# Optimization experiments

Hardware: AMD Instinct MI355X
Metric: run time of the kernel (lower is better)

Reference implementation:

```python
import jax, jax.numpy as jnp
import numpy as np

K = 32                      # nsample (neighbors)
NPTS = [4096, 2048, 1024]   # npts // downsample_ratios [1,2,4]
CH = [(6, 64, 64), (134, 128, 128), (262, 256, 256)]  # (c_in_edge, c_mid, c_out) per EdgeConv
OUT_CH = 128
EPS = 1e-5


def setup_inputs():
    key = jax.random.key(0)
    ks = iter(jax.random.split(key, 64))
    d = {"pcd": jax.random.normal(next(ks), (8, 4096, 3), dtype=jnp.float32)}
    for li, (cin, cmid, cout) in enumerate(CH, start=1):
        d[f"W{li}a"] = jax.random.normal(next(ks), (cmid, cin), dtype=jnp.float32) * 0.05
        d[f"b{li}a"] = jax.random.normal(next(ks), (cmid,), dtype=jnp.float32) * 0.01
        d[f"g{li}a"] = jnp.ones((cmid,), dtype=jnp.float32)
        d[f"be{li}a"] = jnp.zeros((cmid,), dtype=jnp.float32)
        d[f"W{li}b"] = jax.random.normal(next(ks), (cout, cmid), dtype=jnp.float32) * 0.05
        d[f"b{li}b"] = jax.random.normal(next(ks), (cout,), dtype=jnp.float32) * 0.01
        d[f"g{li}b"] = jnp.ones((cout,), dtype=jnp.float32)
        d[f"be{li}b"] = jnp.zeros((cout,), dtype=jnp.float32)
    d["fcW"] = jax.random.normal(next(ks), (OUT_CH, CH[-1][2]), dtype=jnp.float32) * 0.05
    d["fcb"] = jnp.zeros((OUT_CH,), dtype=jnp.float32)
    return d


def _knn_idx(q, p, k):
    # q: [B,m,3] queries, p: [B,n,3] points -> [B,m,k] nearest-neighbor indices
    d = (jnp.sum(q * q, -1)[:, :, None] + jnp.sum(p * p, -1)[:, None, :]
         - 2.0 * jnp.einsum('bmd,bnd->bmn', q, p))
    _, idx = jax.lax.top_k(-d, k)
    return idx


def _bn(x, g, b):
    # training-mode BatchNorm2d over [B,C,m,k], biased variance (torch behavior)
    mu = jnp.mean(x, axis=(0, 2, 3), keepdims=True)
    var = jnp.mean((x - mu) ** 2, axis=(0, 2, 3), keepdims=True)
    return (x - mu) * jax.lax.rsqrt(var + EPS) * g[None, :, None, None] + b[None, :, None, None]


def _edge_conv(xyz, feat, npoints, params):
    # xyz: [B,n,3], feat: [B,C,n] or None. Range sampling = first npoints points.
    W1, b1, g1, be1, W2, b2, g2, be2 = params
    new_xyz = xyz[:, :npoints]
    # use_xyz=True: concat features (as [B,n,C]) with xyz
    f = xyz if feat is None else jnp.concatenate([jnp.transpose(feat, (0, 2, 1)), xyz], -1)
    new_f = f[:, :npoints]                       # [B,m,D]
    idx = _knn_idx(new_xyz, xyz, K)              # [B,m,K]
    knn_f = jax.vmap(lambda a, i: a[i])(f, idx)  # [B,m,K,D] gather
    tiled = jnp.broadcast_to(new_f[:, :, None, :], knn_f.shape)
    e = jnp.concatenate([knn_f - tiled, tiled], -1)  # [B,m,K,2D] edge features
    h = jnp.einsum('bmkc,oc->bomk', e, W1) + b1[None, :, None, None]
    h = jax.nn.relu(_bn(h, g1, be1))
    h = jnp.einsum('bcmk,oc->bomk', h, W2) + b2[None, :, None, None]
    h = jax.nn.relu(_bn(h, g2, be2))
    return new_xyz, jnp.max(h, axis=-1)          # max-pool over K -> [B,C,m]


def reference(pcd, W1a, b1a, g1a, be1a, W1b, b1b, g1b, be1b,
              W2a, b2a, g2a, be2a, W2b, b2b, g2b, be2b,
              W3a, b3a, g3a, be3a, W3b, b3b, g3b, be3b, fcW, fcb):
    xyz = pcd[..., :3]
    feat = None  # pcd has only xyz channels
    layer_params = [
        (W1a, b1a, g1a, be1a, W1b, b1b, g1b, be1b),
        (W2a, b2a, g2a, be2a, W2b, b2b, g2b, be2b),
        (W3a, b3a, g3a, be3a, W3b, b3b, g3b, be3b),
    ]
    for npoints, p in zip(NPTS, layer_params):
        xyz, feat = _edge_conv(xyz, feat, npoints, p)
    out_feat = jnp.einsum('bcn,oc->bon', feat, fcW) + fcb[None, :, None]
    # Range sampling: idx chain of aranges composes to arange(NPTS[-1])
    idx = jnp.broadcast_to(jnp.arange(NPTS[-1]), (pcd.shape[0], NPTS[-1]))
    return xyz, out_feat, idx, feat
```

## Files before the change

### kernel.cpp

```cpp
#include <hip/hip_runtime.h>
#include <hip/hip_bf16.h>

#define B8 8
#define KNN 32
typedef unsigned short u16;
typedef unsigned int u32;
typedef unsigned long long u64;

typedef __attribute__((ext_vector_type(8))) _Float16 half8;
typedef __attribute__((ext_vector_type(4))) float f32x4;

static __device__ __forceinline__ u16 f2h_u(float f) {
  _Float16 h = (_Float16)f; u16 u; __builtin_memcpy(&u, &h, 2); return u;
}
static __device__ __forceinline__ float h2f_u(u16 u) {
  _Float16 h; __builtin_memcpy(&h, &u, 2); return (float)h;
}

static __device__ __forceinline__ u64 enc_key(float d, int id) {
  u32 u = __float_as_uint(d);
  u = (d >= 0.f) ? (u | 0x80000000u) : ~u;
  return ((u64)u << 32) | (u32)id;
}
static __device__ __forceinline__ float dec_val(u64 k) {
  u32 u = (u32)(k >> 32);
  u = (u & 0x80000000u) ? (u & 0x7fffffffu) : ~u;
  return __uint_as_float(u);
}

static __device__ __forceinline__ u64 rank64(u64 mk, int lane, u64* slk, u64* outk, float& tau) {
  slk[lane] = mk;
  int r = 0;
#pragma unroll 16
  for (int j = 0; j < 64; ++j) r += (slk[j] < mk) ? 1 : 0;
  outk[r] = mk;
  u64 res = outk[lane];
  tau = dec_val(outk[31]);
  return res;
}

static __device__ __forceinline__ void bn_from_red(int o, const float* red_s, const float* red_q,
                                                   const float* g, const float* be, float invcnt,
                                                   float* scs, float* shs) {
  float s = 0.f, q = 0.f;
#pragma unroll
  for (int i = 0; i < 16; ++i) { s += red_s[i * 256 + o]; q += red_q[i * 256 + o]; }
  float mu  = s * invcnt;
  float var = fmaxf(q * invcnt - mu * mu, 0.f);
  float scv = g[o] * rsqrtf(var + 1e-5f);
  scs[o] = scv;
  shs[o] = fmaf(-mu, scv, be[o]);
}

__global__ __launch_bounds__(256) void knn_dual(const float* __restrict__ pcd,
                                                int* __restrict__ idx1, int* __restrict__ idx3) {
  __shared__ float4 pts[1024];
  __shared__ u64 bufk[4][32];
  __shared__ u64 slk[4][64];
  __shared__ u64 outk[4][64];
  const int t = threadIdx.x;
  const int lane = t & 63, w = t >> 6;
  const int b = blockIdx.y;
  int N, M, bx; int* idxout;
  if (blockIdx.x < 1024) { N = 4096; M = 4096; bx = blockIdx.x; idxout = idx1; }
  else                   { N = 2048; M = 1024; bx = blockIdx.x - 1024; idxout = idx3; }
  const int m = bx * 4 + w;
  const float* base = pcd + (size_t)b * 12288;
  const float qx = base[m*3], qy = base[m*3+1], qz = base[m*3+2];
  const float ax = -2.f*qx, ay = -2.f*qy, az = -2.f*qz;

  u64 heldk; float tau; int cnt = 0;

  for (int i = t; i < 1024; i += 256) {
    const float* p = base + (size_t)i * 3;
    float x = p[0], y = p[1], z = p[2];
    pts[i] = make_float4(x, y, z, x*x + y*y + z*z);
  }
  __syncthreads();

  {
    float4 p = pts[lane];
    float r0 = fmaf(ax, p.x, fmaf(ay, p.y, fmaf(az, p.z, p.w)));
    heldk = rank64(enc_key(r0, lane), lane, slk[w], outk[w], tau);
  }

  for (int n0 = 0; n0 < N; n0 += 1024) {
    if (n0) {
      __syncthreads();
      for (int i = t; i < 1024; i += 256) {
        const float* p = base + (size_t)(n0 + i) * 3;
        float x = p[0], y = p[1], z = p[2];
        pts[i] = make_float4(x, y, z, x*x + y*y + z*z);
      }
      __syncthreads();
    }
    for (int c = 0; c < 1024; c += 256) {
      float4 p0 = pts[c + lane];
      float4 p1 = pts[c + 64 + lane];
      float4 p2 = pts[c + 128 + lane];
      float4 p3 = pts[c + 192 + lane];
      float r[4];
      r[0] = fmaf(ax, p0.x, fmaf(ay, p0.y, fmaf(az, p0.z, p0.w)));
      r[1] = fmaf(ax, p1.x, fmaf(ay, p1.y, fmaf(az, p1.z, p1.w)));
      r[2] = fmaf(ax, p2.x, fmaf(ay, p2.y, fmaf(az, p2.z, p2.w)));
      r[3] = fmaf(ax, p3.x, fmaf(ay, p3.y, fmaf(az, p3.z, p3.w)));
      if (n0 == 0 && c == 0) r[0] = 3.4e38f;
      float rmn = fminf(fminf(r[0], r[1]), fminf(r[2], r[3]));
      if (!__any(rmn < tau)) continue;
#pragma unroll
      for (int j = 0; j < 4; ++j) {
        float rr = r[j];
        if (!__any(rr < tau)) continue;
        int gid = n0 + c + j * 64 + lane;
        bool pass = rr < tau;
        while (__any(pass)) {
          u64 mk_ = __ballot(pass);
          int before = __popcll(mk_ & ((1ull << lane) - 1ull));
          int total  = __popcll(mk_);
          int room = 32 - cnt;
          if (pass && before < room) {
            bufk[w][cnt + before] = enc_key(rr, gid);
            pass = false;
          }
          if (total >= room) {
            u64 mk = (lane < 32) ? heldk : bufk[w][lane - 32];
            heldk = rank64(mk, lane, slk[w], outk[w], tau);
            cnt = 0;
            pass = pass && (rr < tau);
          } else {
            cnt += total;
          }
        }
      }
    }
  }
  if (cnt > 0) {
    int bl = lane - 32;
    u64 mk = (lane < 32) ? heldk
             : ((bl < cnt) ? bufk[w][bl]
                           : ((0xFFFFFFFFull << 32) | (0xFFFFFF00u | (u32)lane)));
    heldk = rank64(mk, lane, slk[w], outk[w], tau);
  }
  if (lane < KNN) idxout[((size_t)b * M + m) * KNN + lane] = (int)(u32)(heldk & 0xFFFFFFFFu);
}

__global__ void prep_all(
    const float* __restrict__ W1a, const float* __restrict__ W1b,
    const float* __restrict__ W2a, const float* __restrict__ W2b,
    const float* __restrict__ W3a, const float* __restrict__ W3b,
    float* __restrict__ RED,
    float* __restrict__ WAT1, float* __restrict__ WBT1, u16* __restrict__ WBH1,
    float* __restrict__ WBT2, u16* __restrict__ WAH2, u16* __restrict__ WBH2,
    float* __restrict__ WBT3, u16* __restrict__ WAH3, u16* __restrict__ WBH3)
{
  int i0 = blockIdx.x * 256 + threadIdx.x;
  int NT = gridDim.x * 256;
  for (int i = i0; i < 49152; i += NT) RED[i] = 0.f;
  for (int i = i0; i < 256; i += NT) {
    int c = i >> 6, o = i & 63;
    float w1 = (c < 3) ? W1a[o*6 + c] : 0.f;
    float w2 = (c < 3) ? W1a[o*6 + 3 + c] : 0.f;
    WAT1[i] = w1; WBT1[i] = w2 - w1;
  }
  for (int i = i0; i < 4096; i += NT) WBH1[i] = f2h_u(W1b[i]);
  for (int i = i0; i < 68*128; i += NT) {
    int c = i >> 7, o = i & 127;
    float w1 = 0.f, w2 = 0.f;
    if (c < 67) { w1 = W2a[o*134 + c]; w2 = W2a[o*134 + 67 + c]; }
    WBT2[i] = w2 - w1;
  }
  for (int i = i0; i < 128*128; i += NT) {
    int o = i >> 7, k = i & 127;
    WAH2[i] = (k < 67) ? f2h_u(W2a[o*134 + k]) : (u16)0;
  }
  for (int i = i0; i < 16384; i += NT) WBH2[i] = f2h_u(W2b[i]);
  for (int i = i0; i < 132*256; i += NT) {
    int c = i >> 8, o = i & 255;
    float w1 = 0.f, w2 = 0.f;
    if (c < 131) { w1 = W3a[o*262 + c]; w2 = W3a[o*262 + 131 + c]; }
    WBT3[i] = w2 - w1;
  }
  for (int i = i0; i < 256*192; i += NT) {
    int o = i / 192, k = i - o * 192;
    WAH3[i] = (k < 131) ? f2h_u(W3a[o*262 + k]) : (u16)0;
  }
  for (int i = i0; i < 65536; i += NT) WBH3[i] = f2h_u(W3b[i]);
}

template<int C2, int CM, int MODE, int F16>
__global__ __launch_bounds__(256) void conv_a_gemm(
    const void* __restrict__ F, int frs, size_t fbstride,
    const int* __restrict__ idx,
    const float* __restrict__ Wt,
    const float* __restrict__ bias,
    const float* __restrict__ T,
    float* __restrict__ Tout,
    float* __restrict__ red_s, float* __restrict__ red_q,
    int M)
{
  constexpr int KP = (C2 + 3) & ~3;
  constexpr int KC = (KP <= 68) ? KP : 44;
  __shared__ float At[64][KC];
  __shared__ float Wts[KC][64];
  __shared__ int ji[64];
  __shared__ float sred[4][64];
  __shared__ float qred[4][64];
  const int t = threadIdx.x;
  const int rt = blockIdx.x, ot = blockIdx.y, b = blockIdx.z;
  const int R0 = rt * 64, oc0 = ot * 64;

  if (t < 64) {
    int gr = R0 + t;
    ji[t] = (MODE == 0) ? gr : idx[((size_t)b * M + (gr >> 5)) * KNN + (gr & 31)];
  }

  const int cg = t & 15, rg = t >> 4;
  const int r0 = rg * 4, c0 = cg * 4;
  float acc[4][4];
  if (MODE == 0) {
#pragma unroll
    for (int j = 0; j < 4; ++j) {
      float bv = bias[oc0 + c0 + j];
#pragma unroll
      for (int i = 0; i < 4; ++i) acc[i][j] = bv;
    }
  } else {
#pragma unroll
    for (int i = 0; i < 4; ++i) {
      const float* tp = T + ((size_t)b * M + (size_t)((R0 + r0 + i) >> 5)) * CM + oc0 + c0;
      acc[i][0] = tp[0]; acc[i][1] = tp[1]; acc[i][2] = tp[2]; acc[i][3] = tp[3];
    }
  }
  __syncthreads();

  for (int k0 = 0; k0 < KP; k0 += KC) {
    if (k0) __syncthreads();
    for (int i = t; i < KC * 64; i += 256) {
      int c = i >> 6, o = i & 63;
      Wts[c][o] = Wt[(size_t)(k0 + c) * CM + oc0 + o];
    }
    if constexpr (C2 == 3) {
      const float* Fb = (const float*)F + (size_t)b * fbstride;
      for (int i = t; i < 64 * 4; i += 256) {
        int r = i >> 2, c = i & 3;
        At[r][c] = (c < 3) ? Fb[(size_t)ji[r] * 3 + c] : 0.f;
      }
    } else if constexpr (F16) {
      const u16* Fb = (const u16*)F + (size_t)b * fbstride;
      constexpr int C4 = KC / 4;
      for (int i = t; i < 64 * C4; i += 256) {
        int r = i / C4, c4 = i - r * C4;
        ushort4 v = *(const ushort4*)&Fb[(size_t)ji[r] * frs + k0 + c4 * 4];
        At[r][c4*4]   = h2f_u(v.x);
        At[r][c4*4+1] = h2f_u(v.y);
        At[r][c4*4+2] = h2f_u(v.z);
        At[r][c4*4+3] = h2f_u(v.w);
      }
    } else {
      const float* Fb = (const float*)F + (size_t)b * fbstride;
      constexpr int C4 = KC / 4;
      for (int i = t; i < 64 * C4; i += 256) {
        int r = i / C4, c4 = i - r * C4;
        *(float4*)&At[r][c4 * 4] = *(const float4*)&Fb[(size_t)ji[r] * frs + k0 + c4 * 4];
      }
    }
    __syncthreads();

#pragma unroll 4
    for (int k = 0; k < KC; ++k) {
      const float4 w4 = *(const float4*)&Wts[k][c0];
      float a0 = At[r0][k], a1 = At[r0+1][k], a2 = At[r0+2][k], a3 = At[r0+3][k];
      acc[0][0]=fmaf(a0,w4.x,acc[0][0]); acc[0][1]=fmaf(a0,w4.y,acc[0][1]);
      acc[0][2]=fmaf(a0,w4.z,acc[0][2]); acc[0][3]=fmaf(a0,w4.w,acc[0][3]);
      acc[1][0]=fmaf(a1,w4.x,acc[1][0]); acc[1][1]=fmaf(a1,w4.y,acc[1][1]);
      acc[1][2]=fmaf(a1,w4.z,acc[1][2]); acc[1][3]=fmaf(a1,w4.w,acc[1][3]);
      acc[2][0]=fmaf(a2,w4.x,acc[2][0]); acc[2][1]=fmaf(a2,w4.y,acc[2][1]);
      acc[2][2]=fmaf(a2,w4.z,acc[2][2]); acc[2][3]=fmaf(a2,w4.w,acc[2][3]);
      acc[3][0]=fmaf(a3,w4.x,acc[3][0]); acc[3][1]=fmaf(a3,w4.y,acc[3][1]);
      acc[3][2]=fmaf(a3,w4.z,acc[3][2]); acc[3][3]=fmaf(a3,w4.w,acc[3][3]);
    }
  }

  if (MODE == 0) {
    float* op = Tout + ((size_t)b * M + R0) * (size_t)CM + oc0;
#pragma unroll
    for (int i = 0; i < 4; ++i) {
      float* p = op + (size_t)(r0 + i) * CM + c0;
      p[0]=acc[i][0]; p[1]=acc[i][1]; p[2]=acc[i][2]; p[3]=acc[i][3];
    }
  } else {
    float cs[4], cq_[4];
#pragma unroll
    for (int j = 0; j < 4; ++j) {
      float s = acc[0][j] + acc[1][j] + acc[2][j] + acc[3][j];
      float q = acc[0][j]*acc[0][j] + acc[1][j]*acc[1][j] + acc[2][j]*acc[2][j] + acc[3][j]*acc[3][j];
      s += __shfl_xor(s, 16); q += __shfl_xor(q, 16);
      s += __shfl_xor(s, 32); q += __shfl_xor(q, 32);
      cs[j] = s; cq_[j] = q;
    }
    const int wv = t >> 6;
    if ((t & 48) == 0) {
#pragma unroll
      for (int j = 0; j < 4; ++j) { sred[wv][c0 + j] = cs[j]; qred[wv][c0 + j] = cq_[j]; }
    }
    __syncthreads();
    if (t < 64) {
      float s = sred[0][t] + sred[1][t] + sred[2][t] + sred[3][t];
      float q = qred[0][t] + qred[1][t] + qred[2][t] + qred[3][t];
      int shdw = (rt & 15) * 256;
      atomicAdd(&red_s[shdw + t], s);
      atomicAdd(&red_q[shdw + t], q);
    }
  }
}

__global__ __launch_bounds__(256) void l1_convb(
    const float* __restrict__ pcd,
    const int* __restrict__ idx,
    const float* __restrict__ WAT,
    const float* __restrict__ T,
    const u16* __restrict__ Wbh,
    const float* __restrict__ bb,
    const float* __restrict__ gA, const float* __restrict__ beA,
    const float* __restrict__ redA_s, const float* __restrict__ redA_q,
    float* __restrict__ redB_s, float* __restrict__ redB_q,
    float* __restrict__ hmax)
{
  __shared__ u16 Alds[64][72];
  __shared__ u16 Wlds[64][72];
  __shared__ float xyzs[64][4];
  __shared__ float was[3][64];
  __shared__ float scs[64], shs[64];
  __shared__ int ji[64];
  const int t = threadIdx.x;
  const int lane = t & 63, w = t >> 6;
  const int wr = w >> 1, wc = w & 1;
  const int cl = lane & 15, rq = lane >> 4;
  const int rt = blockIdx.x, b = blockIdx.y;
  const int R0 = rt * 64;
  const float* pb = pcd + (size_t)b * 12288;

  if (t < 64) ji[t] = idx[((size_t)b * 4096 + ((R0 + t) >> 5)) * KNN + ((R0 + t) & 31)];
  if (t < 192) was[t / 64][t & 63] = WAT[t];
  if (t >= 192) bn_from_red(t - 192, redA_s, redA_q, gA, beA, 1.f/1048576.f, scs, shs);
  for (int i = t; i < 64 * 8; i += 256) {
    int o = i >> 3, seg = i & 7;
    *(float4*)&Wlds[o][seg * 8] = *(const float4*)&Wbh[(size_t)o * 64 + seg * 8];
  }
  __syncthreads();
  if (t < 64) {
    const float* p = pb + (size_t)ji[t] * 3;
    xyzs[t][0] = p[0]; xyzs[t][1] = p[1]; xyzs[t][2] = p[2]; xyzs[t][3] = 0.f;
  }
  __syncthreads();

  for (int i = t; i < 64 * 8; i += 256) {
    int r = i >> 3, seg = i & 7;
    float px = xyzs[r][0], py = xyzs[r][1], pz = xyzs[r][2];
    const float* Tm = T + ((size_t)b * 4096 + (size_t)((R0 + r) >> 5)) * 64;
    half8 ov;
#pragma unroll
    for (int j2 = 0; j2 < 8; ++j2) {
      int c = seg * 8 + j2;
      float hh = Tm[c];
      hh = fmaf(px, was[0][c], hh);
      hh = fmaf(py, was[1][c], hh);
      hh = fmaf(pz, was[2][c], hh);
      ov[j2] = (_Float16)fmaxf(0.f, fmaf(hh, scs[c], shs[c]));
    }
    *(half8*)&Alds[r][seg * 8] = ov;
  }
  __syncthreads();

  f32x4 acc[2][2];
#pragma unroll
  for (int fr = 0; fr < 2; ++fr)
#pragma unroll
    for (int fc = 0; fc < 2; ++fc) {
      float bv = bb[wc * 32 + fc * 16 + cl];
#pragma unroll
      for (int r = 0; r < 4; ++r) acc[fr][fc][r] = bv;
    }

#pragma unroll
  for (int kk = 0; kk < 2; ++kk) {
    half8 af[2], bf[2];
#pragma unroll
    for (int fr = 0; fr < 2; ++fr)
      af[fr] = *(const half8*)&Alds[wr*32 + fr*16 + cl][kk*32 + rq*8];
#pragma unroll
    for (int fc = 0; fc < 2; ++fc)
      bf[fc] = *(const half8*)&Wlds[wc*32 + fc*16 + cl][kk*32 + rq*8];
#pragma unroll
    for (int fr = 0; fr < 2; ++fr)
#pragma unroll
      for (int fc = 0; fc < 2; ++fc)
        acc[fr][fc] = __builtin_amdgcn_mfma_f32_16x16x32_f16(af[fr], bf[fc], acc[fr][fc], 0, 0, 0);
  }

#pragma unroll
  for (int fc = 0; fc < 2; ++fc) {
    float s = 0.f, q = 0.f, mx = -3.4e38f;
#pragma unroll
    for (int fr = 0; fr < 2; ++fr)
#pragma unroll
      for (int r = 0; r < 4; ++r) {
        float v = acc[fr][fc][r];
        s += v; q += v * v; mx = fmaxf(mx, v);
      }
    s += __shfl_xor(s, 16); q += __shfl_xor(q, 16); mx = fmaxf(mx, __shfl_xor(mx, 16));
    s += __shfl_xor(s, 32); q += __shfl_xor(q, 32); mx = fmaxf(mx, __shfl_xor(mx, 32));
    if (rq == 0) {
      int col = wc * 32 + fc * 16 + cl;
      int shdw = (rt & 15) * 256;
      atomicAdd(&redB_s[shdw + col], s);
      atomicAdd(&redB_q[shdw + col], q);
      hmax[((size_t)b * 4096 + (size_t)(rt * 2 + wr)) * 64 + col] = mx;
    }
  }
}

template<int CM, int KPAD>
__global__ __launch_bounds__(256) void conv_a_mfma(
    const u16* __restrict__ F, int frs, size_t fbstride,
    const int* __restrict__ idx, int idxstride,
    const u16* __restrict__ Wh,
    const float* __restrict__ T,
    u32* __restrict__ H32,
    float* __restrict__ red_s, float* __restrict__ red_q,
    int M)
{
  constexpr int FC = CM / 32;
  __shared__ u16 Alds[64][72];
  __shared__ u16 Wlds[CM][72];
  __shared__ int ji[64];
  const int t = threadIdx.x;
  const int lane = t & 63, w = t >> 6;
  const int wr = w >> 1, wc = w & 1;
  const int cl = lane & 15, rq = lane >> 4;
  const int rt = blockIdx.x, b = blockIdx.y;
  const int R0 = rt * 64;
  const u16* Fb = F + (size_t)b * fbstride;

  if (t < 64) ji[t] = idx[((size_t)b * idxstride + ((R0 + t) >> 5)) * KNN + ((R0 + t) & 31)];

  f32x4 acc[2][FC];
#pragma unroll
  for (int fr = 0; fr < 2; ++fr)
#pragma unroll
    for (int fc = 0; fc < FC; ++fc) {
      int col = wc * (CM/2) + fc * 16 + cl;
#pragma unroll
      for (int r = 0; r < 4; ++r) {
        int row = R0 + wr*32 + fr*16 + rq*4 + r;
        acc[fr][fc][r] = T[((size_t)b * M + (row >> 5)) * CM + col];
      }
    }
  __syncthreads();

  for (int k0 = 0; k0 < KPAD; k0 += 64) {
    if (k0) __syncthreads();
    for (int i = t; i < 64 * 16; i += 256) {
      int r = i >> 4, seg = i & 15;
      int k = k0 + seg * 4;
      ushort4 s = {0,0,0,0};
      if (k < frs) s = *(const ushort4*)&Fb[(size_t)ji[r] * frs + k];
      *(ushort4*)&Alds[r][seg * 4] = s;
    }
    for (int i = t; i < CM * 8; i += 256) {
      int o = i >> 3, seg = i & 7;
      *(float4*)&Wlds[o][seg * 8] = *(const float4*)&Wh[(size_t)o * KPAD + k0 + seg * 8];
    }
    __syncthreads();

#pragma unroll
    for (int kk = 0; kk < 2; ++kk) {
      half8 af[2], bf[FC];
#pragma unroll
      for (int fr = 0; fr < 2; ++fr)
        af[fr] = *(const half8*)&Alds[wr*32 + fr*16 + cl][kk*32 + rq*8];
#pragma unroll
      for (int fc = 0; fc < FC; ++fc)
        bf[fc] = *(const half8*)&Wlds[wc*(CM/2) + fc*16 + cl][kk*32 + rq*8];
#pragma unroll
      for (int fr = 0; fr < 2; ++fr)
#pragma unroll
        for (int fc = 0; fc < FC; ++fc)
          acc[fr][fc] = __builtin_amdgcn_mfma_f32_16x16x32_f16(af[fr], bf[fc], acc[fr][fc], 0, 0, 0);
    }
  }

  u32* Hb4 = H32 + ((size_t)b * ((size_t)M * KNN / 4) + (size_t)(R0 >> 2)) * CM;
#pragma unroll
  for (int fr = 0; fr < 2; ++fr)
#pragma unroll
    for (int fc = 0; fc < FC; ++fc) {
      int col = wc*(CM/2) + fc*16 + cl;
      u32 v = __builtin_amdgcn_cvt_pk_fp8_f32(acc[fr][fc][0], acc[fr][fc][1], 0, false);
      v = __builtin_amdgcn_cvt_pk_fp8_f32(acc[fr][fc][2], acc[fr][fc][3], v, true);
      Hb4[(size_t)(wr*8 + fr*4 + rq) * CM + col] = v;
    }

#pragma unroll
  for (int fc = 0; fc < FC; ++fc) {
    float s = 0.f, q = 0.f;
#pragma unroll
    for (int fr = 0; fr < 2; ++fr)
#pragma unroll
      for (int r = 0; r < 4; ++r) {
        float v = acc[fr][fc][r];
        s += v; q += v * v;
      }
    s += __shfl_xor(s, 16); q += __shfl_xor(q, 16);
    s += __shfl_xor(s, 32); q += __shfl_xor(q, 32);
    if (rq == 0) {
      int col = wc*(CM/2) + fc*16 + cl;
      int shdw = (rt & 15) * 256;
      atomicAdd(&red_s[shdw + col], s);
      atomicAdd(&red_q[shdw + col], q);
    }
  }
}

template<int CM>
__global__ __launch_bounds__(512) void conv_b_fused(
    const u32* __restrict__ H32,
    const u16* __restrict__ Wh,
    const float* __restrict__ bb,
    const float* __restrict__ gA, const float* __restrict__ beA,
    const float* __restrict__ redA_s, const float* __restrict__ redA_q, float invcnt,
    float* __restrict__ redB_s, float* __restrict__ redB_q,
    float* __restrict__ hmax,
    int Mrows)
{
  constexpr int FC = CM / 32;
  __shared__ u16 Alds[128][72];
  __shared__ u16 Wlds[CM][72];
  __shared__ float scs[CM], shs[CM];
  const int t = threadIdx.x;
  const int lane = t & 63, w = t >> 6;
  const int wr = w >> 1;
  const int wc = w & 1;
  const int cl = lane & 15, rq = lane >> 4;
  const int rt = blockIdx.x, b = blockIdx.y;
  const u32* Hb4 = H32 + ((size_t)b * ((size_t)Mrows / 4) + (size_t)(rt * 32)) * CM;

  for (int i = t; i < CM; i += 512) bn_from_red(i, redA_s, redA_q, gA, beA, invcnt, scs, shs);

  f32x4 acc[2][FC];
#pragma unroll
  for (int fr = 0; fr < 2; ++fr)
#pragma unroll
    for (int fc = 0; fc < FC; ++fc) {
      float bv = bb[wc * (CM/2) + fc * 16 + cl];
#pragma unroll
      for (int r = 0; r < 4; ++r) acc[fr][fc][r] = bv;
    }
  __syncthreads();

  for (int k0 = 0; k0 < CM; k0 += 64) {
    if (k0) __syncthreads();
    for (int i = t; i < 128 * 8; i += 512) {
      int r = i >> 3, seg = i & 7;
      int rg = r >> 2, sh8 = (r & 3) * 8;
      const u32* hp = Hb4 + (size_t)rg * CM + k0 + seg * 8;
      half8 ov;
#pragma unroll
      for (int j = 0; j < 8; ++j) {
        float v = __builtin_amdgcn_cvt_f32_fp8((hp[j] >> sh8) & 0xffu, 0);
        int c = k0 + seg * 8 + j;
        v = fmaxf(0.f, fmaf(v, scs[c], shs[c]));
        ov[j] = (_Float16)v;
      }
      *(half8*)&Alds[r][seg * 8] = ov;
    }
    for (int i = t; i < CM * 8; i += 512) {
      int o = i >> 3, seg = i & 7;
      *(float4*)&Wlds[o][seg * 8] = *(const float4*)&Wh[(size_t)o * CM + k0 + seg * 8];
    }
    __syncthreads();

#pragma unroll
    for (int kk = 0; kk < 2; ++kk) {
      half8 af[2], bf[FC];
#pragma unroll
      for (int fr = 0; fr < 2; ++fr)
        af[fr] = *(const half8*)&Alds[wr*32 + fr*16 + cl][kk*32 + rq*8];
#pragma unroll
      for (int fc = 0; fc < FC; ++fc)
        bf[fc] = *(const half8*)&Wlds[wc*(CM/2) + fc*16 + cl][kk*32 + rq*8];
#pragma unroll
      for (int fr = 0; fr < 2; ++fr)
#pragma unroll
        for (int fc = 0; fc < FC; ++fc)
          acc[fr][fc] = __builtin_amdgcn_mfma_f32_16x16x32_f16(af[fr], bf[fc], acc[fr][fc], 0, 0, 0);
    }
  }

#pragma unroll
  for (int fc = 0; fc < FC; ++fc) {
    float s = 0.f, q = 0.f, mx = -3.4e38f;
#pragma unroll
    for (int fr = 0; fr < 2; ++fr)
#pragma unroll
      for (int r = 0; r < 4; ++r) {
        float v = acc[fr][fc][r];
        s += v; q += v * v; mx = fmaxf(mx, v);
      }
    s += __shfl_xor(s, 16); q += __shfl_xor(q, 16); mx = fmaxf(mx, __shfl_xor(mx, 16));
    s += __shfl_xor(s, 32); q += __shfl_xor(q, 32); mx = fmaxf(mx, __shfl_xor(mx, 32));
    if (rq == 0) {
      int col = wc*(CM/2) + fc*16 + cl;
      int shdw = (rt & 15) * 256;
      atomicAdd(&redB_s[shdw + col], s);
      atomicAdd(&redB_q[shdw + col], q);
      hmax[((size_t)b * (Mrows >> 5) + (size_t)(rt * 4 + wr)) * CM + col] = mx;
    }
  }
}

__global__ __launch_bounds__(256) void bnrelu_fb(const float* __restrict__ hm,
    const float* __restrict__ gB, const float* __restrict__ beB,
    const float* __restrict__ redB_s, const float* __restrict__ redB_q, float invcnt,
    const float* __restrict__ pcd,
    u16* __restrict__ fout, int CM, int fostride, size_t fobstride, int M) {
  __shared__ float scs[256], shs[256];
  for (int o = threadIdx.x; o < CM; o += 256) bn_from_red(o, redB_s, redB_q, gB, beB, invcnt, scs, shs);
  __syncthreads();
  int i = blockIdx.x * 256 + threadIdx.x;
  int cq = CM >> 2;
  int total = B8 * M * cq;
  if (i >= total) return;
  int c4 = i % cq; int r = i / cq;
  int b = r / M, m = r - b * M;
  float4 v = *(const float4*)&hm[((size_t)b * M + m) * CM + c4 * 4];
  int c = c4 * 4;
  ushort4 o;
  o.x = f2h_u(fmaxf(0.f, fmaf(v.x, scs[c],   shs[c])));
  o.y = f2h_u(fmaxf(0.f, fmaf(v.y, scs[c+1], shs[c+1])));
  o.z = f2h_u(fmaxf(0.f, fmaf(v.z, scs[c+2], shs[c+2])));
  o.w = f2h_u(fmaxf(0.f, fmaf(v.w, scs[c+3], shs[c+3])));
  u16* op = fout + (size_t)b * fobstride + (size_t)m * fostride;
  *(ushort4*)(op + c) = o;
  if (pcd && c4 == 0) {
    const float* p = pcd + ((size_t)b * 4096 + m) * 3;
    half8 xz;
    xz[0] = (_Float16)p[0]; xz[1] = (_Float16)p[1]; xz[2] = (_Float16)p[2];
    xz[3] = (_Float16)0.f; xz[4] = (_Float16)0.f; xz[5] = (_Float16)0.f;
    xz[6] = (_Float16)0.f; xz[7] = (_Float16)0.f;
    *(half8*)(op + CM) = xz;
  }
}

__global__ __launch_bounds__(256) void fc_fused(
    const float* __restrict__ hm,
    const float* __restrict__ gB, const float* __restrict__ beB,
    const float* __restrict__ redB_s, const float* __restrict__ redB_q, float invcnt,
    const float* __restrict__ fcW, const float* __restrict__ fcb,
    const float* __restrict__ pcd,
    float* __restrict__ out0, float* __restrict__ out1,
    float* __restrict__ out2, float* __restrict__ out3) {
  __shared__ float tile[32 * 257];
  __shared__ float scs[256], shs[256];
  const int t = threadIdx.x, b = blockIdx.x, n0 = blockIdx.y * 32;
  bn_from_red(t, redB_s, redB_q, gB, beB, invcnt, scs, shs);
  __syncthreads();
  for (int i = t; i < 32 * 64; i += 256) {
    int n = i >> 6, c4 = i & 63;
    float4 v = *(const float4*)&hm[((size_t)b * 1024 + n0 + n) * 256 + c4 * 4];
    int c = c4 * 4;
    float* tp = &tile[n * 257 + c];
    tp[0] = fmaxf(0.f, fmaf(v.x, scs[c],   shs[c]));
    tp[1] = fmaxf(0.f, fmaf(v.y, scs[c+1], shs[c+1]));
    tp[2] = fmaxf(0.f, fmaf(v.z, scs[c+2], shs[c+2]));
    tp[3] = fmaxf(0.f, fmaf(v.w, scs[c+3], shs[c+3]));
  }
  __syncthreads();
  const int n = t & 31, og = t >> 5;
#pragma unroll
  for (int ci = 0; ci < 32; ++ci) {
    int c = og * 32 + ci;
    out3[((size_t)b * 256 + c) * 1024 + n0 + n] = tile[n * 257 + c];
  }
#pragma unroll
  for (int oi = 0; oi < 16; ++oi) {
    int o = og * 16 + oi;
    float acc = fcb[o];
    const float* w = fcW + (size_t)o * 256;
#pragma unroll 4
    for (int c = 0; c < 256; ++c) acc = fmaf(tile[n * 257 + c], w[c], acc);
    out1[((size_t)b * 128 + o) * 1024 + n0 + n] = acc;
  }
  if (t < 32) {
    int nn = n0 + t;
    const float* p = pcd + ((size_t)b * 4096 + nn) * 3;
    float* o0 = out0 + ((size_t)b * 1024 + nn) * 3;
    o0[0] = p[0]; o0[1] = p[1]; o0[2] = p[2];
    out2[(size_t)b * 1024 + nn] = (float)nn;
  }
}

extern "C" void kernel_launch(void* const* d_in, const int* in_sizes, int n_in,
                              void* d_out, int out_size, void* d_ws, size_t ws_size,
                              hipStream_t stream) {
  (void)in_sizes; (void)n_in; (void)out_size; (void)ws_size;
  const float* pcd = (const float*)d_in[0];
  const float* W1a = (const float*)d_in[1];  const float* b1a = (const float*)d_in[2];
  const float* g1a = (const float*)d_in[3];  const float* be1a= (const float*)d_in[4];
  const float* W1b = (const float*)d_in[5];  const float* b1b = (const float*)d_in[6];
  const float* g1b = (const float*)d_in[7];  const float* be1b= (const float*)d_in[8];
  const float* W2a = (const float*)d_in[9];  const float* b2a = (const float*)d_in[10];
  const float* g2a = (const float*)d_in[11]; const float* be2a= (const float*)d_in[12];
  const float* W2b = (const float*)d_in[13]; const float* b2b = (const float*)d_in[14];
  const float* g2b = (const float*)d_in[15]; const float* be2b= (const float*)d_in[16];
  const float* W3a = (const float*)d_in[17]; const float* b3a = (const float*)d_in[18];
  const float* g3a = (const float*)d_in[19]; const float* be3a= (const float*)d_in[20];
  const float* W3b = (const float*)d_in[21]; const float* b3b = (const float*)d_in[22];
  const float* g3b = (const float*)d_in[23]; const float* be3b= (const float*)d_in[24];
  const float* fcW = (const float*)d_in[25]; const float* fcb = (const float*)d_in[26];

  u16* FB2h = (u16*)d_ws;
  u16* FB3h = FB2h + 2359296;
  float* wsf = (float*)(FB3h + 2228224);
  float* TBUF= wsf;
  float* RED = TBUF + 2097152;
  float* R1A = RED;          float* R1B = RED + 8192;
  float* R2A = RED + 16384;  float* R2B = RED + 24576;
  float* R3A = RED + 32768;  float* R3B = RED + 40960;
  float* WAT1 = RED + 49152;
  float* WBT1 = WAT1 + 256;
  float* WBT2 = WBT1 + 256;
  float* WBT3 = WBT2 + 8704;
  float* HMAX = WBT3 + 33792;
  int* IDX1 = (int*)(HMAX + 2097152);
  int* IDX3 = IDX1 + (size_t)8 * 4096 * 32;
  u32* H32  = (u32*)(IDX3 + (size_t)8 * 1024 * 32);
  u16* WBH1 = (u16*)(H32 + 16777216);
  u16* WAH2 = WBH1 + 4096;
  u16* WBH2 = WAH2 + 16384;
  u16* WAH3 = WBH2 + 16384;
  u16* WBH3 = WAH3 + 49152;

  float* out0 = (float*)d_out;
  float* out1 = out0 + 24576;
  float* out2 = out1 + 1048576;
  float* out3 = out2 + 8192;

  prep_all<<<64, 256, 0, stream>>>(W1a, W1b, W2a, W2b, W3a, W3b, RED,
                                   WAT1, WBT1, WBH1, WBT2, WAH2, WBH2, WBT3, WAH3, WBH3);

  knn_dual<<<dim3(1280, 8), 256, 0, stream>>>(pcd, IDX1, IDX3);

  conv_a_gemm<3,64,0,0><<<dim3(64,1,8),256,0,stream>>>(pcd,3,(size_t)12288,nullptr,WBT1,b1a,nullptr,TBUF,nullptr,nullptr,4096);
  conv_a_gemm<3,64,1,0><<<dim3(2048,1,8),256,0,stream>>>(pcd,3,(size_t)12288,IDX1,WAT1,nullptr,TBUF,nullptr,R1A,R1A+4096,4096);
  l1_convb<<<dim3(2048,8),256,0,stream>>>(pcd,IDX1,WAT1,TBUF,WBH1,b1b,g1a,be1a,R1A,R1A+4096,R1B,R1B+4096,HMAX);
  bnrelu_fb<<<2048,256,0,stream>>>(HMAX,g1b,be1b,R1B,R1B+4096,1.f/1048576.f,pcd,FB2h,64,72,(size_t)294912,4096);

  conv_a_gemm<67,128,0,1><<<dim3(32,2,8),256,0,stream>>>(FB2h,72,(size_t)294912,nullptr,WBT2,b2a,nullptr,TBUF,nullptr,nullptr,2048);
  conv_a_mfma<128,128><<<dim3(1024,8),256,0,stream>>>(FB2h,72,(size_t)294912,IDX1,4096,WAH2,TBUF,H32,R2A,R2A+4096,2048);
  conv_b_fused<128><<<dim3(512,8),512,0,stream>>>(H32,WBH2,b2b,g2a,be2a,R2A,R2A+4096,1.f/524288.f,R2B,R2B+4096,HMAX,2048*32);
  bnrelu_fb<<<2048,256,0,stream>>>(HMAX,g2b,be2b,R2B,R2B+4096,1.f/524288.f,pcd,FB3h,128,136,(size_t)278528,2048);

  conv_a_gemm<131,256,0,1><<<dim3(16,4,8),256,0,stream>>>(FB3h,136,(size_t)278528,nullptr,WBT3,b3a,nullptr,TBUF,nullptr,nullptr,1024);
  conv_a_mfma<256,192><<<dim3(512,8),256,0,stream>>>(FB3h,136,(size_t)278528,IDX3,1024,WAH3,TBUF,H32,R3A,R3A+4096,1024);
  conv_b_fused<256><<<dim3(256,8),512,0,stream>>>(H32,WBH3,b3b,g3a,be3a,R3A,R3A+4096,1.f/262144.f,R3B,R3B+4096,HMAX,1024*32);

  fc_fused<<<dim3(8, 32), 256, 0, stream>>>(HMAX,g3b,be3b,R3B,R3B+4096,1.f/262144.f,fcW,fcb,pcd,out0,out1,out2,out3);
}
```

Before: 730.9 us.

## Fuse layer-1 BN-A statistics into the KNN kernel, drop separate gather GEMM

The layer-1 first-conv statistics pass (a gathered GEMM over 2048x8 blocks computing sum and sum-of-squares) is folded into the tail of the KNN kernel. Each wave now uses its freshly selected neighbor indices to compute h = T + W·p_neighbor per channel, reducing into shared memory and then into the shadowed global accumulators. The precomputed T GEMM is moved before KNN so the fused kernel can read it. This removes one launch and a re-read of the index buffer, at the cost of extra per-lane scalar gathers and atomics inside the KNN kernel.

```diff
diff --git a/kernel.cpp b/kernel.cpp
--- a/kernel.cpp
+++ b/kernel.cpp
@@ -53,11 +53,15 @@
 }
 
 __global__ __launch_bounds__(256) void knn_dual(const float* __restrict__ pcd,
-                                                int* __restrict__ idx1, int* __restrict__ idx3) {
+                                                int* __restrict__ idx1, int* __restrict__ idx3,
+                                                const float* __restrict__ T,
+                                                const float* __restrict__ WAT1,
+                                                float* __restrict__ red_s, float* __restrict__ red_q) {
   __shared__ float4 pts[1024];
   __shared__ u64 bufk[4][32];
   __shared__ u64 slk[4][64];
   __shared__ u64 outk[4][64];
+  __shared__ float sred[64], qred[64];
   const int t = threadIdx.x;
   const int lane = t & 63, w = t >> 6;
   const int b = blockIdx.y;
@@ -142,6 +146,30 @@
     heldk = rank64(mk, lane, slk[w], outk[w], tau);
   }
   if (lane < KNN) idxout[((size_t)b * M + m) * KNN + lane] = (int)(u32)(heldk & 0xFFFFFFFFu);
+
+  if (t < 64) { sred[t] = 0.f; qred[t] = 0.f; }
+  __syncthreads();
+  if (blockIdx.x < 1024) {
+    float tval = T[((size_t)b * 4096 + m) * 64 + lane];
+    float w0 = WAT1[lane], w1 = WAT1[64 + lane], w2 = WAT1[128 + lane];
+    float s = 0.f, q = 0.f;
+#pragma unroll 4
+    for (int k = 0; k < KNN; ++k) {
+      u64 kk = __shfl(heldk, k);
+      int nk = (int)(u32)kk;
+      const float* p = base + (size_t)nk * 3;
+      float h = fmaf(p[2], w2, fmaf(p[1], w1, fmaf(p[0], w0, tval)));
+      s += h; q += h * h;
+    }
+    atomicAdd(&sred[lane], s);
+    atomicAdd(&qred[lane], q);
+  }
+  __syncthreads();
+  if (blockIdx.x < 1024 && t < 64) {
+    int shdw = (bx & 15) * 256;
+    atomicAdd(&red_s[shdw + t], sred[t]);
+    atomicAdd(&red_q[shdw + t], qred[t]);
+  }
 }
 
 __global__ void prep_all(
@@ -187,51 +215,31 @@
   for (int i = i0; i < 65536; i += NT) WBH3[i] = f2h_u(W3b[i]);
 }
 
-template<int C2, int CM, int MODE, int F16>
+template<int C2, int CM, int F16>
 __global__ __launch_bounds__(256) void conv_a_gemm(
     const void* __restrict__ F, int frs, size_t fbstride,
-    const int* __restrict__ idx,
     const float* __restrict__ Wt,
     const float* __restrict__ bias,
-    const float* __restrict__ T,
     float* __restrict__ Tout,
-    float* __restrict__ red_s, float* __restrict__ red_q,
     int M)
 {
   constexpr int KP = (C2 + 3) & ~3;
   constexpr int KC = (KP <= 68) ? KP : 44;
   __shared__ float At[64][KC];
   __shared__ float Wts[KC][64];
-  __shared__ int ji[64];
-  __shared__ float sred[4][64];
-  __shared__ float qred[4][64];
   const int t = threadIdx.x;
   const int rt = blockIdx.x, ot = blockIdx.y, b = blockIdx.z;
   const int R0 = rt * 64, oc0 = ot * 64;
 
-  if (t < 64) {
-    int gr = R0 + t;
-    ji[t] = (MODE == 0) ? gr : idx[((size_t)b * M + (gr >> 5)) * KNN + (gr & 31)];
-  }
-
   const int cg = t & 15, rg = t >> 4;
   const int r0 = rg * 4, c0 = cg * 4;
   float acc[4][4];
-  if (MODE == 0) {
-#pragma unroll
-    for (int j = 0; j < 4; ++j) {
-      float bv = bias[oc0 + c0 + j];
-#pragma unroll
-      for (int i = 0; i < 4; ++i) acc[i][j] = bv;
-    }
-  } else {
-#pragma unroll
-    for (int i = 0; i < 4; ++i) {
-      const float* tp = T + ((size_t)b * M + (size_t)((R0 + r0 + i) >> 5)) * CM + oc0 + c0;
-      acc[i][0] = tp[0]; acc[i][1] = tp[1]; acc[i][2] = tp[2]; acc[i][3] = tp[3];
-    }
-  }
-  __syncthreads();
+#pragma unroll
+  for (int j = 0; j < 4; ++j) {
+    float bv = bias[oc0 + c0 + j];
+#pragma unroll
+    for (int i = 0; i < 4; ++i) acc[i][j] = bv;
+  }
 
   for (int k0 = 0; k0 < KP; k0 += KC) {
     if (k0) __syncthreads();
@@ -243,25 +251,18 @@
       const float* Fb = (const float*)F + (size_t)b * fbstride;
       for (int i = t; i < 64 * 4; i += 256) {
         int r = i >> 2, c = i & 3;
-        At[r][c] = (c < 3) ? Fb[(size_t)ji[r] * 3 + c] : 0.f;
+        At[r][c] = (c < 3) ? Fb[(size_t)(R0 + r) * 3 + c] : 0.f;
       }
     } else if constexpr (F16) {
       const u16* Fb = (const u16*)F + (size_t)b * fbstride;
       constexpr int C4 = KC / 4;
       for (int i = t; i < 64 * C4; i += 256) {
         int r = i / C4, c4 = i - r * C4;
-        ushort4 v = *(const ushort4*)&Fb[(size_t)ji[r] * frs + k0 + c4 * 4];
+        ushort4 v = *(const ushort4*)&Fb[(size_t)(R0 + r) * frs + k0 + c4 * 4];
         At[r][c4*4]   = h2f_u(v.x);
         At[r][c4*4+1] = h2f_u(v.y);
         At[r][c4*4+2] = h2f_u(v.z);
         At[r][c4*4+3] = h2f_u(v.w);
-      }
-    } else {
-      const float* Fb = (const float*)F + (size_t)b * fbstride;
-      constexpr int C4 = KC / 4;
-      for (int i = t; i < 64 * C4; i += 256) {
-        int r = i / C4, c4 = i - r * C4;
-        *(float4*)&At[r][c4 * 4] = *(const float4*)&Fb[(size_t)ji[r] * frs + k0 + c4 * 4];
       }
     }
     __syncthreads();
@@ -281,36 +282,11 @@
     }
   }
 
-  if (MODE == 0) {
-    float* op = Tout + ((size_t)b * M + R0) * (size_t)CM + oc0;
-#pragma unroll
-    for (int i = 0; i < 4; ++i) {
-      float* p = op + (size_t)(r0 + i) * CM + c0;
-      p[0]=acc[i][0]; p[1]=acc[i][1]; p[2]=acc[i][2]; p[3]=acc[i][3];
-    }
-  } else {
-    float cs[4], cq_[4];
-#pragma unroll
-    for (int j = 0; j < 4; ++j) {
-      float s = acc[0][j] + acc[1][j] + acc[2][j] + acc[3][j];
-      float q = acc[0][j]*acc[0][j] + acc[1][j]*acc[1][j] + acc[2][j]*acc[2][j] + acc[3][j]*acc[3][j];
-      s += __shfl_xor(s, 16); q += __shfl_xor(q, 16);
-      s += __shfl_xor(s, 32); q += __shfl_xor(q, 32);
-      cs[j] = s; cq_[j] = q;
-    }
-    const int wv = t >> 6;
-    if ((t & 48) == 0) {
-#pragma unroll
-      for (int j = 0; j < 4; ++j) { sred[wv][c0 + j] = cs[j]; qred[wv][c0 + j] = cq_[j]; }
-    }
-    __syncthreads();
-    if (t < 64) {
-      float s = sred[0][t] + sred[1][t] + sred[2][t] + sred[3][t];
-      float q = qred[0][t] + qred[1][t] + qred[2][t] + qred[3][t];
-      int shdw = (rt & 15) * 256;
-      atomicAdd(&red_s[shdw + t], s);
-      atomicAdd(&red_q[shdw + t], q);
-    }
+  float* op = Tout + ((size_t)b * M + R0) * (size_t)CM + oc0;
+#pragma unroll
+  for (int i = 0; i < 4; ++i) {
+    float* p = op + (size_t)(r0 + i) * CM + c0;
+    p[0]=acc[i][0]; p[1]=acc[i][1]; p[2]=acc[i][2]; p[3]=acc[i][3];
   }
 }
 
@@ -749,19 +725,18 @@
   prep_all<<<64, 256, 0, stream>>>(W1a, W1b, W2a, W2b, W3a, W3b, RED,
                                    WAT1, WBT1, WBH1, WBT2, WAH2, WBH2, WBT3, WAH3, WBH3);
 
-  knn_dual<<<dim3(1280, 8), 256, 0, stream>>>(pcd, IDX1, IDX3);
-
-  conv_a_gemm<3,64,0,0><<<dim3(64,1,8),256,0,stream>>>(pcd,3,(size_t)12288,nullptr,WBT1,b1a,nullptr,TBUF,nullptr,nullptr,4096);
-  conv_a_gemm<3,64,1,0><<<dim3(2048,1,8),256,0,stream>>>(pcd,3,(size_t)12288,IDX1,WAT1,nullptr,TBUF,nullptr,R1A,R1A+4096,4096);
+  conv_a_gemm<3,64,0><<<dim3(64,1,8),256,0,stream>>>(pcd,3,(size_t)12288,WBT1,b1a,TBUF,4096);
+  knn_dual<<<dim3(1280, 8), 256, 0, stream>>>(pcd, IDX1, IDX3, TBUF, WAT1, R1A, R1A+4096);
+
   l1_convb<<<dim3(2048,8),256,0,stream>>>(pcd,IDX1,WAT1,TBUF,WBH1,b1b,g1a,be1a,R1A,R1A+4096,R1B,R1B+4096,HMAX);
   bnrelu_fb<<<2048,256,0,stream>>>(HMAX,g1b,be1b,R1B,R1B+4096,1.f/1048576.f,pcd,FB2h,64,72,(size_t)294912,4096);
 
-  conv_a_gemm<67,128,0,1><<<dim3(32,2,8),256,0,stream>>>(FB2h,72,(size_t)294912,nullptr,WBT2,b2a,nullptr,TBUF,nullptr,nullptr,2048);
+  conv_a_gemm<67,128,1><<<dim3(32,2,8),256,0,stream>>>(FB2h,72,(size_t)294912,WBT2,b2a,TBUF,2048);
   conv_a_mfma<128,128><<<dim3(1024,8),256,0,stream>>>(FB2h,72,(size_t)294912,IDX1,4096,WAH2,TBUF,H32,R2A,R2A+4096,2048);
   conv_b_fused<128><<<dim3(512,8),512,0,stream>>>(H32,WBH2,b2b,g2a,be2a,R2A,R2A+4096,1.f/524288.f,R2B,R2B+4096,HMAX,2048*32);
   bnrelu_fb<<<2048,256,0,stream>>>(HMAX,g2b,be2b,R2B,R2B+4096,1.f/524288.f,pcd,FB3h,128,136,(size_t)278528,2048);
 
-  conv_a_gemm<131,256,0,1><<<dim3(16,4,8),256,0,stream>>>(FB3h,136,(size_t)278528,nullptr,WBT3,b3a,nullptr,TBUF,nullptr,nullptr,1024);
+  conv_a_gemm<131,256,1><<<dim3(16,4,8),256,0,stream>>>(FB3h,136,(size_t)278528,WBT3,b3a,TBUF,1024);
   conv_a_mfma<256,192><<<dim3(512,8),256,0,stream>>>(FB3h,136,(size_t)278528,IDX3,1024,WAH3,TBUF,H32,R3A,R3A+4096,1024);
   conv_b_fused<256><<<dim3(256,8),512,0,stream>>>(H32,WBH3,b3b,g3a,be3a,R3A,R3A+4096,1.f/262144.f,R3B,R3B+4096,HMAX,1024*32);
 
```

Measured after the change: 732.2 us. No clear change (+0.2%).
